# Kernel tuning notes

Measured on AMD Instinct MI355X. Metric: run time of the kernel, lower is better.

## Reference

```python
import jax, jax.numpy as jnp
import numpy as np

BN_EPS = 1e-5


def maxpool2(x):
    # 2x2 max pool, stride 2: (B,C,H,W) -> (B,C,H//2,W//2)
    B, C, H, W = x.shape
    return x.reshape(B, C, H // 2, 2, W // 2, 2).max(axis=(3, 5))


def setup_inputs() -> dict:
    key = jax.random.key(0)
    ks = jax.random.split(key, 6)
    B, C, H, W = 4, 64, 96, 96   # in_dim = 64
    K, OD = 64, 64               # key_dim, out_dim
    sc = lambda fan: 1.0 / np.sqrt(fan)
    return {
        "c2": jax.random.normal(ks[0], (B, C, H, W), jnp.float32),
        "x": jax.random.normal(ks[1], (B, C, H, W), jnp.float32),
        # edge_att: Conv2d(2C->OD, 1x1, no bias) -> BN -> ReLU -> Conv2d(OD->1, 1x1) -> Sigmoid
        "w_ea1": jax.random.normal(ks[2], (OD, 2 * C), jnp.float32) * sc(2 * C),
        "bn_w": jnp.ones((OD,), jnp.float32),
        "bn_b": jnp.zeros((OD,), jnp.float32),
        "bn_m": jnp.zeros((OD,), jnp.float32),
        "bn_v": jnp.ones((OD,), jnp.float32),
        "w_ea2": jax.random.normal(ks[3], (1, OD), jnp.float32) * sc(OD),
        "b_ea2": jnp.zeros((1,), jnp.float32),
        # query_conv (shared for query AND key in the original forward)
        "w_q": jax.random.normal(ks[4], (K, C), jnp.float32) * sc(C),
        "b_q": jnp.zeros((K,), jnp.float32),
        "gamma": jnp.full((1,), 0.5, jnp.float32),
    }


def reference(c2, x, w_ea1, bn_w, bn_b, bn_m, bn_v, w_ea2, b_ea2, w_q, b_q, gamma):
    xp = maxpool2(x)        # (B,C,Hp,Wp)
    c2p = maxpool2(c2)
    B, C, H, W = x.shape
    Hp, Wp = xp.shape[2], xp.shape[3]

    # edge attention gate on pooled features -> (B,1,Hp,Wp)
    cat = jnp.concatenate([c2p, xp], axis=1)                       # (B,2C,Hp,Wp)
    h = jnp.einsum('oc,bchw->bohw', w_ea1, cat)
    bn_scale = (bn_w / jnp.sqrt(bn_v + BN_EPS))[None, :, None, None]
    h = jax.nn.relu((h - bn_m[None, :, None, None]) * bn_scale + bn_b[None, :, None, None])
    ea = jax.nn.sigmoid(jnp.einsum('oc,bchw->bohw', w_ea2, h) + b_ea2[None, :, None, None])

    # query at full res, key at pooled res (SAME conv weights, as in the source)
    q = jnp.einsum('kc,bchw->bkhw', w_q, x) + b_q[None, :, None, None]    # (B,K,H,W)
    k = jnp.einsum('kc,bchw->bkhw', w_q, xp) + b_q[None, :, None, None]   # (B,K,Hp,Wp)

    pq = q.reshape(B, -1, H * W)        # (B,K,N)
    pk = k.reshape(B, -1, Hp * Wp)      # (B,K,M)
    energy = jnp.einsum('bkn,bkm->bnm', pq, pk)                    # (B,N,M)
    attn = jax.nn.softmax(energy * ea.reshape(B, 1, Hp * Wp), axis=-1)

    v = xp.reshape(B, C, Hp * Wp)                                   # (B,C,M)
    out = jnp.einsum('bcm,bnm->bcn', v, attn).reshape(B, C, H, W)
    return gamma[0] * out + x
```

## Files before the change

kernel.cpp:

```cpp
#include <hip/hip_runtime.h>
#include <stdint.h>

#define B_ 4
#define C_ 64
#define H_ 96
#define W_ 96
#define HP_ 48
#define WP_ 48
#define N_ (H_*W_)
#define M_ (HP_*WP_)
#define KD_ 64
#define OD_ 64
#define BN_EPS 1e-5f
#define LOG2E 1.4426950408889634f
#define SHIFT2 28.853900817779268f
#define QT_ 48
#define QI_ (QT_/16)
#define QB_ (N_/QT_)
#define NT_ (M_/64)

typedef __bf16 bf16_t;
typedef bf16_t bf16x8 __attribute__((ext_vector_type(8)));
typedef bf16_t bf16x4 __attribute__((ext_vector_type(4)));
typedef float f32x4 __attribute__((ext_vector_type(4)));
typedef short short4v __attribute__((ext_vector_type(4)));

static __device__ __forceinline__ unsigned short f2bf(float f) {
    unsigned int u = __builtin_bit_cast(unsigned int, f);
    u += 0x7fffu + ((u >> 16) & 1u);
    return (unsigned short)(u >> 16);
}

static __device__ __forceinline__ f32x4 mfma16_bf16(short4v a, short4v b, f32x4 c) {
#if __has_builtin(__builtin_amdgcn_mfma_f32_16x16x16bf16_1k)
    return __builtin_amdgcn_mfma_f32_16x16x16bf16_1k(a, b, c, 0, 0, 0);
#else
    return c;
#endif
}

static __device__ __forceinline__ void gl_lds16(const unsigned short* g, unsigned short* l) {
#if __has_builtin(__builtin_amdgcn_global_load_lds)
    __builtin_amdgcn_global_load_lds(
        (const __attribute__((address_space(1))) unsigned int*)(const void*)g,
        (__attribute__((address_space(3))) unsigned int*)(void*)l, 16, 0, 0);
#endif
}

static __device__ __forceinline__ void setprio1() {
#if __has_builtin(__builtin_amdgcn_s_setprio)
    __builtin_amdgcn_s_setprio(1);
#endif
}
static __device__ __forceinline__ void setprio0() {
#if __has_builtin(__builtin_amdgcn_s_setprio)
    __builtin_amdgcn_s_setprio(0);
#endif
}
static __device__ __forceinline__ void schedbar0() {
#if __has_builtin(__builtin_amdgcn_sched_barrier)
    __builtin_amdgcn_sched_barrier(0);
#endif
}
static __device__ __forceinline__ void rawbar() {
#if __has_builtin(__builtin_amdgcn_s_barrier)
    __builtin_amdgcn_s_barrier();
#else
    __syncthreads();
#endif
}

__global__ __launch_bounds__(256) void prep_kernel(
    const float* __restrict__ x, const float* __restrict__ c2,
    const float* __restrict__ wq, const float* __restrict__ bq,
    const float* __restrict__ w1, const float* __restrict__ bnw, const float* __restrict__ bnb,
    const float* __restrict__ bnm, const float* __restrict__ bnv,
    const float* __restrict__ w2, const float* __restrict__ b2,
    unsigned short* __restrict__ kb, unsigned short* __restrict__ vb, float* __restrict__ ea) {

    __shared__ float lw1[OD_*2*C_];
    __shared__ float lwq[KD_*C_];
    __shared__ float xs[C_*33];
    __shared__ float c2s[C_*33];
    __shared__ float red[8][32];

    int tid = threadIdx.x;
    int b = blockIdx.x / 72;
    int m0 = (blockIdx.x % 72) * 32;

    for (int i = tid; i < OD_*2*C_; i += 256) lw1[i] = w1[i];
    for (int i = tid; i < KD_*C_; i += 256) lwq[i] = wq[i];
    for (int j = tid; j < 2048; j += 256) {
        int c = j >> 5, p = j & 31;
        int m = m0 + p;
        int hp = m / WP_, wp = m % WP_;
        size_t base = ((size_t)(b*C_ + c)*H_ + 2*hp)*W_ + 2*wp;
        const float* px = x + base;
        float mx = fmaxf(fmaxf(px[0], px[1]), fmaxf(px[W_], px[W_+1]));
        xs[c*33 + p] = mx;
        vb[(size_t)(b*C_ + c)*M_ + m] = f2bf(mx);
        const float* pc = c2 + base;
        c2s[c*33 + p] = fmaxf(fmaxf(pc[0], pc[1]), fmaxf(pc[W_], pc[W_+1]));
    }
    __syncthreads();

    int ml = tid & 31, oz = tid >> 5;
    int m = m0 + ml;

    float h[8] = {0,0,0,0,0,0,0,0};
    for (int c = 0; c < C_; c += 4) {
        float x0 = xs[c*33+ml], x1 = xs[(c+1)*33+ml], x2 = xs[(c+2)*33+ml], x3 = xs[(c+3)*33+ml];
        #pragma unroll
        for (int oi = 0; oi < 8; oi++) {
            const float4 wv = *(const float4*)&lwq[(oz*8 + oi)*C_ + c];
            h[oi] = fmaf(wv.x, x0, fmaf(wv.y, x1, fmaf(wv.z, x2, fmaf(wv.w, x3, h[oi]))));
        }
    }
    unsigned short tmp[8];
    #pragma unroll
    for (int oi = 0; oi < 8; oi++) tmp[oi] = f2bf(h[oi] + bq[oz*8 + oi]);
    *(uint4*)&kb[((size_t)b*M_ + m)*KD_ + oz*8] = *(const uint4*)tmp;

    float g[8] = {0,0,0,0,0,0,0,0};
    for (int c = 0; c < 2*C_; c += 4) {
        const float* srcb = (c < C_) ? &c2s[c*33] : &xs[(c - C_)*33];
        float x0 = srcb[ml], x1 = srcb[33+ml], x2 = srcb[66+ml], x3 = srcb[99+ml];
        #pragma unroll
        for (int oi = 0; oi < 8; oi++) {
            const float4 wv = *(const float4*)&lw1[(oz*8 + oi)*(2*C_) + c];
            g[oi] = fmaf(wv.x, x0, fmaf(wv.y, x1, fmaf(wv.z, x2, fmaf(wv.w, x3, g[oi]))));
        }
    }
    float z = 0.f;
    #pragma unroll
    for (int oi = 0; oi < 8; oi++) {
        int o = oz*8 + oi;
        float sc = bnw[o] * rsqrtf(bnv[o] + BN_EPS);
        float t = (g[oi] - bnm[o]) * sc + bnb[o];
        z += w2[o] * fmaxf(t, 0.f);
    }
    red[oz][ml] = z;
    __syncthreads();
    if (oz == 0) {
        float s = b2[0];
        #pragma unroll
        for (int i = 0; i < 8; i++) s += red[i][ml];
        ea[(size_t)b*M_ + m] = LOG2E / (1.f + __builtin_amdgcn_exp2f(-s * LOG2E));
    }
}

__global__ __launch_bounds__(256) void qk_kernel(const float* __restrict__ in, const float* __restrict__ wq,
    const float* __restrict__ bq, unsigned short* __restrict__ outb) {
    __shared__ float lw[KD_*C_];
    for (int i = threadIdx.x; i < KD_*C_; i += 256) lw[i] = wq[i];
    __syncthreads();
    int ml = threadIdx.x & 31, oz = threadIdx.x >> 5;
    int pg = blockIdx.x * 32 + ml;
    float h[8] = {0,0,0,0,0,0,0,0};
    const float* src = in + ((size_t)(pg / N_))*C_*N_ + (pg % N_);
    for (int c = 0; c < C_; c += 4) {
        float x0 = src[(size_t)c*N_], x1 = src[(size_t)(c+1)*N_];
        float x2 = src[(size_t)(c+2)*N_], x3 = src[(size_t)(c+3)*N_];
        #pragma unroll
        for (int oi = 0; oi < 8; oi++) {
            const float4 wv = *(const float4*)&lw[(oz*8 + oi)*C_ + c];
            h[oi] = fmaf(wv.x, x0, fmaf(wv.y, x1, fmaf(wv.z, x2, fmaf(wv.w, x3, h[oi]))));
        }
    }
    unsigned short tmp[8];
    #pragma unroll
    for (int oi = 0; oi < 8; oi++) tmp[oi] = f2bf(h[oi] + bq[oz*8 + oi]);
    *(uint4*)&outb[(size_t)pg*KD_ + oz*8] = *(const uint4*)tmp;
}

__global__ __launch_bounds__(256, 3) void attn_kernel(
    const unsigned short* __restrict__ qb, const unsigned short* __restrict__ kb,
    const unsigned short* __restrict__ vb, const float* __restrict__ ea,
    const float* __restrict__ x, const float* __restrict__ gamma_p, float* __restrict__ out) {

    __shared__ __align__(16) char smem[41984];

    int tid = threadIdx.x;
    int wave = tid >> 6, lane = tid & 63, quad = lane >> 4, l16 = lane & 15;
    int blk = blockIdx.x;
    int b = (blk & 7) >> 1;
    int n_base = ((blk & 1) * (QB_/2) + (blk >> 3)) * QT_;

    bf16x8 qf[QI_][2];
    #pragma unroll
    for (int qi = 0; qi < QI_; qi++) {
        const unsigned short* qp = qb + ((size_t)b*N_ + n_base + qi*16 + l16)*KD_;
        qf[qi][0] = __builtin_bit_cast(bf16x8, *(const uint4*)(qp + quad*8));
        qf[qi][1] = __builtin_bit_cast(bf16x8, *(const uint4*)(qp + 32 + quad*8));
    }

    f32x4 o2[QI_][4];
    f32x4 lacc[QI_];
    #pragma unroll
    for (int qi = 0; qi < QI_; qi++) {
        lacc[qi] = (f32x4){0.f,0.f,0.f,0.f};
        #pragma unroll
        for (int ct = 0; ct < 4; ct++) o2[qi][ct] = (f32x4){0.f,0.f,0.f,0.f};
    }
    const short one_bf = (short)0x3F80;
    short4v ones = (short4v){one_bf, one_bf, one_bf, one_bf};

    const unsigned short* kbB = kb + (size_t)b*M_*KD_;
    const unsigned short* vbB = vb + (size_t)b*C_*M_;
    const float* eaB = ea + (size_t)b*M_;

    int srow = tid >> 3;
    int ksw  = ((tid & 7) ^ (srow & 7)) << 3;

    auto STAGE = [&](int mb, char* kd, char* vd) {
        unsigned short* kds = (unsigned short*)kd;
        unsigned short* vds = (unsigned short*)vd;
        gl_lds16(kbB + (size_t)(mb + srow)*KD_      + ksw, kds + tid*8);
        gl_lds16(kbB + (size_t)(mb + srow + 32)*KD_ + ksw, kds + 2048 + tid*8);
        gl_lds16(vbB + (size_t)srow*M_      + mb + ksw, vds + tid*8);
        gl_lds16(vbB + (size_t)(srow+32)*M_ + mb + ksw, vds + 2048 + tid*8);
    };

    {
        const f32x4* eaV = (const f32x4*)eaB;
        f32x4* eaL = (f32x4*)(smem + 32768);
        for (int i = tid; i < M_/4; i += 256) eaL[i] = eaV[i];
    }
    STAGE(0,  smem,          smem + 8192);
    STAGE(64, smem + 16384,  smem + 16384 + 8192);
    asm volatile("s_waitcnt lgkmcnt(0)" ::: "memory");

    const float* lds_ea = (const float*)(smem + 32768);
    int xsw = l16 & 7;

    for (int mt = 0; mt < NT_; mt++) {
        int cur = mt & 1;
        if (mt < NT_ - 1) { asm volatile("s_waitcnt vmcnt(4)" ::: "memory"); }
        else             { asm volatile("s_waitcnt vmcnt(0)" ::: "memory"); }
        rawbar();

        unsigned short* kc = (unsigned short*)(smem + cur*16384);
        unsigned short* vc = (unsigned short*)(smem + cur*16384 + 8192);

        f32x4 e4 = *(const f32x4*)&lds_ea[mt*64 + wave*16 + quad*4];
        int krow = wave*16 + l16;
        bf16x8 kf0 = __builtin_bit_cast(bf16x8, *(const uint4*)(kc + krow*KD_ + (((quad  ) ^ xsw) << 3)));
        bf16x8 kf1 = __builtin_bit_cast(bf16x8, *(const uint4*)(kc + krow*KD_ + (((quad+4) ^ xsw) << 3)));
        short4v va[4];
        #pragma unroll
        for (int ct = 0; ct < 4; ct++)
            va[ct] = *(const short4v*)(vc + (ct*16 + l16)*64
                        + (((wave*2 + (quad>>1)) ^ xsw) << 3) + (quad&1)*4);

        asm volatile("s_waitcnt lgkmcnt(0)" ::: "memory");
        rawbar();
        schedbar0();

        if (mt < NT_ - 2) {
            char* nb = smem + cur*16384;
            STAGE((mt+2)*64, nb, nb + 8192);
        }

        f32x4 st[QI_];
        setprio1();
        #pragma unroll
        for (int qi = 0; qi < QI_; qi++) {
            f32x4 z = (f32x4){0.f,0.f,0.f,0.f};
            z = __builtin_amdgcn_mfma_f32_16x16x32_bf16(kf0, qf[qi][0], z, 0, 0, 0);
            z = __builtin_amdgcn_mfma_f32_16x16x32_bf16(kf1, qf[qi][1], z, 0, 0, 0);
            st[qi] = z;
        }
        setprio0();

        short4v pk[QI_];
        #pragma unroll
        for (int qi = 0; qi < QI_; qi++) {
            f32x4 p;
            p[0] = __builtin_amdgcn_exp2f(fmaf(st[qi][0], e4[0], -SHIFT2));
            p[1] = __builtin_amdgcn_exp2f(fmaf(st[qi][1], e4[1], -SHIFT2));
            p[2] = __builtin_amdgcn_exp2f(fmaf(st[qi][2], e4[2], -SHIFT2));
            p[3] = __builtin_amdgcn_exp2f(fmaf(st[qi][3], e4[3], -SHIFT2));
            pk[qi] = __builtin_bit_cast(short4v, __builtin_convertvector(p, bf16x4));
        }

        setprio1();
        #pragma unroll
        for (int ct = 0; ct < 4; ct++)
            #pragma unroll
            for (int qi = 0; qi < QI_; qi++)
                o2[qi][ct] = mfma16_bf16(va[ct], pk[qi], o2[qi][ct]);
        #pragma unroll
        for (int qi = 0; qi < QI_; qi++)
            lacc[qi] = mfma16_bf16(ones, pk[qi], lacc[qi]);
        setprio0();
    }

    float* o_red0 = (float*)smem;
    float* o_red1 = o_red0 + QT_*68;
    float* l_red  = o_red1 + QT_*68;

    if (lane < 16) {
        #pragma unroll
        for (int qi = 0; qi < QI_; qi++) l_red[wave*QT_ + qi*16 + l16] = lacc[qi][0];
    }
    if (wave < 2) {
        float* od = (wave == 0) ? o_red0 : o_red1;
        #pragma unroll
        for (int qi = 0; qi < QI_; qi++)
            #pragma unroll
            for (int ct = 0; ct < 4; ct++)
                *(f32x4*)&od[(qi*16 + l16)*68 + ct*16 + quad*4] = o2[qi][ct];
    }
    __syncthreads();
    if (wave >= 2) {
        float* od = (wave == 2) ? o_red0 : o_red1;
        #pragma unroll
        for (int qi = 0; qi < QI_; qi++)
            #pragma unroll
            for (int ct = 0; ct < 4; ct++) {
                f32x4* p = (f32x4*)&od[(qi*16 + l16)*68 + ct*16 + quad*4];
                *p += o2[qi][ct];
            }
    }
    __syncthreads();
    if (tid < QT_) {
        float s = (l_red[tid] + l_red[QT_ + tid]) + (l_red[2*QT_ + tid] + l_red[3*QT_ + tid]);
        l_red[tid] = 1.f / s;
    }
    __syncthreads();

    float gmm = gamma_p[0];
    int c = tid >> 2, q4 = tid & 3;
    const float* xrow = x + ((size_t)b*C_ + c)*N_ + n_base;
    float* orow = out + ((size_t)b*C_ + c)*N_ + n_base;
    #pragma unroll
    for (int i = 0; i < QI_; i++) {
        int q0 = q4*4 + i*16;
        float4 xv = *(const float4*)(xrow + q0);
        float4 ov;
        float v0 = (o_red0[(q0+0)*68 + c] + o_red1[(q0+0)*68 + c]) * l_red[q0+0];
        float v1 = (o_red0[(q0+1)*68 + c] + o_red1[(q0+1)*68 + c]) * l_red[q0+1];
        float v2 = (o_red0[(q0+2)*68 + c] + o_red1[(q0+2)*68 + c]) * l_red[q0+2];
        float v3 = (o_red0[(q0+3)*68 + c] + o_red1[(q0+3)*68 + c]) * l_red[q0+3];
        ov.x = fmaf(gmm, v0, xv.x);
        ov.y = fmaf(gmm, v1, xv.y);
        ov.z = fmaf(gmm, v2, xv.z);
        ov.w = fmaf(gmm, v3, xv.w);
        *(float4*)(orow + q0) = ov;
    }
}

extern "C" void kernel_launch(void* const* d_in, const int* in_sizes, int n_in,
                              void* d_out, int out_size, void* d_ws, size_t ws_size,
                              hipStream_t stream) {
    const float* c2    = (const float*)d_in[0];
    const float* x     = (const float*)d_in[1];
    const float* w_ea1 = (const float*)d_in[2];
    const float* bn_w  = (const float*)d_in[3];
    const float* bn_b  = (const float*)d_in[4];
    const float* bn_m  = (const float*)d_in[5];
    const float* bn_v  = (const float*)d_in[6];
    const float* w_ea2 = (const float*)d_in[7];
    const float* b_ea2 = (const float*)d_in[8];
    const float* w_q   = (const float*)d_in[9];
    const float* b_q   = (const float*)d_in[10];
    const float* gamma = (const float*)d_in[11];
    float* out = (float*)d_out;

    char* ws = (char*)d_ws;
    float* ea            = (float*)(ws + 0);
    unsigned short* qb   = (unsigned short*)(ws + 36864);
    unsigned short* kb   = (unsigned short*)(ws + 4755456);
    unsigned short* vb   = (unsigned short*)(ws + 5935104);

    prep_kernel<<<dim3((B_*M_)/32), dim3(256), 0, stream>>>(x, c2, w_q, b_q,
        w_ea1, bn_w, bn_b, bn_m, bn_v, w_ea2, b_ea2, kb, vb, ea);
    qk_kernel<<<dim3((B_*N_)/32), dim3(256), 0, stream>>>(x, w_q, b_q, qb);
    attn_kernel<<<dim3(B_*QB_), dim3(256), 0, stream>>>(qb, kb, vb, ea, x, gamma, out);
}
```

Before: 163.1 us.

## Double-buffer K/V LDS fragments in registers across attention tiles

Rewrites the attention main loop as a 2x-unrolled macro with two register fragment sets. The LDS reads of K, V and the edge-attention values for the next tile are issued before the current tile's MFMAs, and only the older reads are waited on. This is meant to hide LDS read latency behind the QK, exp and PV matrix work. In exchange it raises register pressure and changes the global wait to vmcnt(0) once per step. It also adds a trailing __syncthreads before the reduction.

```diff
diff --git a/kernel.cpp b/kernel.cpp
--- a/kernel.cpp
+++ b/kernel.cpp
@@ -228,72 +228,100 @@
     }
     STAGE(0,  smem,          smem + 8192);
     STAGE(64, smem + 16384,  smem + 16384 + 8192);
+    asm volatile("s_waitcnt vmcnt(4)" ::: "memory");
     asm volatile("s_waitcnt lgkmcnt(0)" ::: "memory");
+    rawbar();
+    asm volatile("" ::: "memory");
 
     const float* lds_ea = (const float*)(smem + 32768);
     int xsw = l16 & 7;
-
-    for (int mt = 0; mt < NT_; mt++) {
-        int cur = mt & 1;
-        if (mt < NT_ - 1) { asm volatile("s_waitcnt vmcnt(4)" ::: "memory"); }
-        else             { asm volatile("s_waitcnt vmcnt(0)" ::: "memory"); }
-        rawbar();
-
-        unsigned short* kc = (unsigned short*)(smem + cur*16384);
-        unsigned short* vc = (unsigned short*)(smem + cur*16384 + 8192);
-
-        f32x4 e4 = *(const f32x4*)&lds_ea[mt*64 + wave*16 + quad*4];
-        int krow = wave*16 + l16;
-        bf16x8 kf0 = __builtin_bit_cast(bf16x8, *(const uint4*)(kc + krow*KD_ + (((quad  ) ^ xsw) << 3)));
-        bf16x8 kf1 = __builtin_bit_cast(bf16x8, *(const uint4*)(kc + krow*KD_ + (((quad+4) ^ xsw) << 3)));
-        short4v va[4];
-        #pragma unroll
-        for (int ct = 0; ct < 4; ct++)
-            va[ct] = *(const short4v*)(vc + (ct*16 + l16)*64
-                        + (((wave*2 + (quad>>1)) ^ xsw) << 3) + (quad&1)*4);
-
-        asm volatile("s_waitcnt lgkmcnt(0)" ::: "memory");
-        rawbar();
-        schedbar0();
-
-        if (mt < NT_ - 2) {
-            char* nb = smem + cur*16384;
-            STAGE((mt+2)*64, nb, nb + 8192);
-        }
-
-        f32x4 st[QI_];
-        setprio1();
-        #pragma unroll
-        for (int qi = 0; qi < QI_; qi++) {
-            f32x4 z = (f32x4){0.f,0.f,0.f,0.f};
-            z = __builtin_amdgcn_mfma_f32_16x16x32_bf16(kf0, qf[qi][0], z, 0, 0, 0);
-            z = __builtin_amdgcn_mfma_f32_16x16x32_bf16(kf1, qf[qi][1], z, 0, 0, 0);
-            st[qi] = z;
-        }
-        setprio0();
-
-        short4v pk[QI_];
-        #pragma unroll
-        for (int qi = 0; qi < QI_; qi++) {
-            f32x4 p;
-            p[0] = __builtin_amdgcn_exp2f(fmaf(st[qi][0], e4[0], -SHIFT2));
-            p[1] = __builtin_amdgcn_exp2f(fmaf(st[qi][1], e4[1], -SHIFT2));
-            p[2] = __builtin_amdgcn_exp2f(fmaf(st[qi][2], e4[2], -SHIFT2));
-            p[3] = __builtin_amdgcn_exp2f(fmaf(st[qi][3], e4[3], -SHIFT2));
-            pk[qi] = __builtin_bit_cast(short4v, __builtin_convertvector(p, bf16x4));
-        }
-
-        setprio1();
-        #pragma unroll
-        for (int ct = 0; ct < 4; ct++)
-            #pragma unroll
-            for (int qi = 0; qi < QI_; qi++)
-                o2[qi][ct] = mfma16_bf16(va[ct], pk[qi], o2[qi][ct]);
-        #pragma unroll
-        for (int qi = 0; qi < QI_; qi++)
-            lacc[qi] = mfma16_bf16(ones, pk[qi], lacc[qi]);
-        setprio0();
-    }
+    int krow = wave*16 + l16;
+
+    struct FragSet { bf16x8 kf0, kf1; short4v va0, va1, va2, va3; f32x4 e4; };
+    FragSet fA, fB;
+
+    {
+        unsigned short* kc = (unsigned short*)smem;
+        unsigned short* vc = (unsigned short*)(smem + 8192);
+        fA.e4  = *(const f32x4*)&lds_ea[0*64 + wave*16 + quad*4];
+        fA.kf0 = __builtin_bit_cast(bf16x8, *(const uint4*)(kc + krow*KD_ + (((quad  ) ^ xsw) << 3)));
+        fA.kf1 = __builtin_bit_cast(bf16x8, *(const uint4*)(kc + krow*KD_ + (((quad+4) ^ xsw) << 3)));
+        fA.va0 = *(const short4v*)(vc + (0*16 + l16)*64 + (((wave*2 + (quad>>1)) ^ xsw) << 3) + (quad&1)*4);
+        fA.va1 = *(const short4v*)(vc + (1*16 + l16)*64 + (((wave*2 + (quad>>1)) ^ xsw) << 3) + (quad&1)*4);
+        fA.va2 = *(const short4v*)(vc + (2*16 + l16)*64 + (((wave*2 + (quad>>1)) ^ xsw) << 3) + (quad&1)*4);
+        fA.va3 = *(const short4v*)(vc + (3*16 + l16)*64 + (((wave*2 + (quad>>1)) ^ xsw) << 3) + (quad&1)*4);
+    }
+
+#define ATTN_STEP(T_, CUR, NXT)                                                        \
+    {                                                                                  \
+        const int t_ = (T_);                                                           \
+        if (t_ < NT_ - 1) {                                                            \
+            asm volatile("s_waitcnt vmcnt(0)" ::: "memory");   \
+            schedbar0();                                                               \
+            rawbar();                                \
+            asm volatile("" ::: "memory");                                             \
+            schedbar0();                                                               \
+            if (t_ + 2 < NT_) {                                                        \
+                char* nb = smem + (t_ & 1) * 16384;                                    \
+                STAGE((t_ + 2) * 64, nb, nb + 8192);                                   \
+            }                                                                          \
+            unsigned short* kc_ = (unsigned short*)(smem + ((t_ + 1) & 1) * 16384);    \
+            unsigned short* vc_ = (unsigned short*)(smem + ((t_ + 1) & 1) * 16384 + 8192); \
+            NXT.e4  = *(const f32x4*)&lds_ea[(t_ + 1)*64 + wave*16 + quad*4];          \
+            NXT.kf0 = __builtin_bit_cast(bf16x8, *(const uint4*)(kc_ + krow*KD_ + (((quad  ) ^ xsw) << 3))); \
+            NXT.kf1 = __builtin_bit_cast(bf16x8, *(const uint4*)(kc_ + krow*KD_ + (((quad+4) ^ xsw) << 3))); \
+            NXT.va0 = *(const short4v*)(vc_ + (0*16 + l16)*64 + (((wave*2 + (quad>>1)) ^ xsw) << 3) + (quad&1)*4); \
+            NXT.va1 = *(const short4v*)(vc_ + (1*16 + l16)*64 + (((wave*2 + (quad>>1)) ^ xsw) << 3) + (quad&1)*4); \
+            NXT.va2 = *(const short4v*)(vc_ + (2*16 + l16)*64 + (((wave*2 + (quad>>1)) ^ xsw) << 3) + (quad&1)*4); \
+            NXT.va3 = *(const short4v*)(vc_ + (3*16 + l16)*64 + (((wave*2 + (quad>>1)) ^ xsw) << 3) + (quad&1)*4); \
+            schedbar0();                                                               \
+            asm volatile("s_waitcnt lgkmcnt(7)" ::: "memory");   \
+            schedbar0();                                                               \
+        } else {                                                                       \
+            schedbar0();                                                               \
+            asm volatile("s_waitcnt lgkmcnt(0)" ::: "memory");      \
+            schedbar0();                                                               \
+        }                                                                              \
+                               \
+        f32x4 st[QI_];                                                                 \
+        setprio1();                                                                    \
+        _Pragma("unroll")                                                              \
+        for (int qi = 0; qi < QI_; qi++) {                                             \
+            f32x4 z = (f32x4){0.f,0.f,0.f,0.f};                                        \
+            z = __builtin_amdgcn_mfma_f32_16x16x32_bf16(CUR.kf0, qf[qi][0], z, 0, 0, 0); \
+            z = __builtin_amdgcn_mfma_f32_16x16x32_bf16(CUR.kf1, qf[qi][1], z, 0, 0, 0); \
+            st[qi] = z;                                                                \
+        }                                                                              \
+        setprio0();                                                                    \
+        short4v pk[QI_];                                                               \
+        _Pragma("unroll")                                                              \
+        for (int qi = 0; qi < QI_; qi++) {                                             \
+            f32x4 p;                                                                   \
+            p[0] = __builtin_amdgcn_exp2f(fmaf(st[qi][0], CUR.e4[0], -SHIFT2));        \
+            p[1] = __builtin_amdgcn_exp2f(fmaf(st[qi][1], CUR.e4[1], -SHIFT2));        \
+            p[2] = __builtin_amdgcn_exp2f(fmaf(st[qi][2], CUR.e4[2], -SHIFT2));        \
+            p[3] = __builtin_amdgcn_exp2f(fmaf(st[qi][3], CUR.e4[3], -SHIFT2));        \
+            pk[qi] = __builtin_bit_cast(short4v, __builtin_convertvector(p, bf16x4));  \
+        }                                                                              \
+        setprio1();                                                                    \
+        _Pragma("unroll")                                                              \
+        for (int qi = 0; qi < QI_; qi++) {                                             \
+            o2[qi][0] = mfma16_bf16(CUR.va0, pk[qi], o2[qi][0]);                       \
+            o2[qi][1] = mfma16_bf16(CUR.va1, pk[qi], o2[qi][1]);                       \
+            o2[qi][2] = mfma16_bf16(CUR.va2, pk[qi], o2[qi][2]);                       \
+            o2[qi][3] = mfma16_bf16(CUR.va3, pk[qi], o2[qi][3]);                       \
+            lacc[qi]  = mfma16_bf16(ones,    pk[qi], lacc[qi]);                        \
+        }                                                                              \
+        setprio0();                                                                    \
+    }
+
+    for (int t = 0; t < NT_; t += 2) {
+        ATTN_STEP(t,     fA, fB);
+        ATTN_STEP(t + 1, fB, fA);
+    }
+#undef ATTN_STEP
+
+    __syncthreads();
 
     float* o_red0 = (float*)smem;
     float* o_red1 = o_red0 + QT_*68;
```

Result: no change. 160.6 us (-1.5%).
